# Kernel optimization log

Hardware: AMD Instinct MI355X
Metric: run time of the kernel (lower is better)

Reference implementation:

```python
import jax, jax.numpy as jnp
import numpy as np

B, V, H, E, Q = 32768, 2048, 256, 16, 4  # batch, num_visible, hidden_dim, num_experts, num_qubits
ENERGY_SCALE = 3.0
T_INIT, T_FINAL, N_STEPS = 1.0, 0.1, 100
SEED = 1  # annealing_counter after one call


def setup_inputs() -> dict:
    key = jax.random.key(0)
    ks = jax.random.split(key, 6)
    x = jax.random.normal(ks[0], (B, V), jnp.float32)
    We = jax.random.normal(ks[1], (V, H), jnp.float32) / np.sqrt(V).astype(np.float32)
    be = jnp.zeros((H,), jnp.float32)
    W1 = jax.random.normal(ks[2], (H + E, Q), jnp.float32) / np.sqrt(H + E).astype(np.float32)
    b1 = jnp.zeros((Q,), jnp.float32)
    w2 = jax.random.normal(ks[3], (Q,), jnp.float32) / np.sqrt(Q).astype(np.float32)
    b2 = jnp.zeros((), jnp.float32)
    inv_temp = jnp.ones((), jnp.float32)  # initial_inverse_temp = 1.0
    return dict(x=x, We=We, be=be, W1=W1, b1=b1, w2=w2, b2=b2, inv_temp=inv_temp)


def _energies(x, We, be, W1, b1, w2, b2):
    # feature_encoder: Dense(H, tanh)
    enc = jnp.tanh(x @ We + be)                       # [B, H]
    # combined = concat([enc tiled over experts, one_hot(expert)], -1) -> energy MLP.
    # one_hot @ W1[H:] just selects rows, so split the matmul instead of tiling:
    W1e, W1i = W1[:H], W1[H:]                         # [H,Q], [E,Q]
    h = jnp.tanh(enc @ W1e[None] if False else jnp.tanh((enc @ W1e)[:, None, :] + W1i[None, :, :] + b1))  # [B,E,Q]
    energies = ENERGY_SCALE * jnp.tanh(jnp.einsum('beq,q->be', h, w2) + b2)  # [B, E]
    return energies


def _qbm_sample(energies, seed):
    # Annealed Metropolis-Hastings over experts, geometric temperature schedule.
    key = jax.random.key(seed)
    kinit, kloop = jax.random.split(key)
    cur = jax.random.randint(kinit, (B,), 0, E)
    log_ratio = jnp.log(jnp.float32(T_FINAL / T_INIT))

    def step(cur, t):
        kt = jax.random.fold_in(kloop, t)
        kp, ku = jax.random.split(kt)
        frac = t.astype(jnp.float32) / jnp.float32(N_STEPS - 1)
        T = jnp.float32(T_INIT) * jnp.exp(log_ratio * frac)
        prop = jax.random.randint(kp, (B,), 0, E)
        e_prop = jnp.take_along_axis(energies, prop[:, None], 1)[:, 0]
        e_cur = jnp.take_along_axis(energies, cur[:, None], 1)[:, 0]
        accept = jax.random.uniform(ku, (B,)) < jnp.exp(jnp.minimum((e_cur - e_prop) / T, 0.0) + 0.0) * jnp.exp(jnp.minimum(-(e_prop - e_cur) / T, 0.0) * 0.0)
        # standard MH: accept if u < exp(-dE/T) (auto-accepts dE<=0)
        accept = jax.random.uniform(jax.random.fold_in(ku, 1), (B,)) < jnp.exp(jnp.minimum(-(e_prop - e_cur) / T, 0.0))
        return jnp.where(accept, prop, cur), None

    cur, _ = jax.lax.scan(step, cur, jnp.arange(N_STEPS))
    logp = jax.nn.log_softmax(-energies / jnp.float32(T_FINAL), axis=-1)
    sample_log_probs = jnp.take_along_axis(logp, cur[:, None], 1)[:, 0]
    final_e = jnp.take_along_axis(energies, cur[:, None], 1)[:, 0]
    return cur, sample_log_probs, final_e


def reference(x, We, be, W1, b1, w2, b2, inv_temp):
    energies = _energies(x, We, be, W1, b1, w2, b2)   # [B, E]
    beta = jax.nn.softplus(inv_temp)
    logits = -beta * energies
    # training=True, use_annealing=True path: stochastic expert selection
    assignments, _slp, _ae = _qbm_sample(jax.lax.stop_gradient(energies), SEED)
    probabilities = jax.nn.one_hot(assignments, E, dtype=jnp.float32)
    return probabilities, energies, logits
```

## Files before the change

kernel.cpp:

```cpp
#include <hip/hip_runtime.h>
#include <math.h>
#include <stdint.h>

#define B_N 32768
#define V_N 2048
#define H_N 256
#define E_N 16
#define Q_N 4

#define KT 64
#define NSTRIP (V_N/KT)
#define BROWS 32
#define KG_N (V_N/8)
#define NSS (V_N/128)

#define RNG_PART 1

typedef double f64x4 __attribute__((ext_vector_type(4)));
typedef float  f32x4 __attribute__((ext_vector_type(4)));
typedef short  bf16x8 __attribute__((ext_vector_type(8)));

union U8 { unsigned u[4]; bf16x8 v; };

#define TF_R(x0,x1,r) { x0 += x1; x1 = ((x1 << (r)) | (x1 >> (32-(r)))); x1 ^= x0; }

__device__ __forceinline__ void tf_block(uint32_t k0, uint32_t k1, uint32_t &x0, uint32_t &x1){
  uint32_t k2 = k0 ^ k1 ^ 0x1BD11BDAu;
  x0 += k0; x1 += k1;
  TF_R(x0,x1,13) TF_R(x0,x1,15) TF_R(x0,x1,26) TF_R(x0,x1,6)
  x0 += k1; x1 += k2 + 1u;
  TF_R(x0,x1,17) TF_R(x0,x1,29) TF_R(x0,x1,16) TF_R(x0,x1,24)
  x0 += k2; x1 += k0 + 2u;
  TF_R(x0,x1,13) TF_R(x0,x1,15) TF_R(x0,x1,26) TF_R(x0,x1,6)
  x0 += k0; x1 += k1 + 3u;
  TF_R(x0,x1,17) TF_R(x0,x1,29) TF_R(x0,x1,16) TF_R(x0,x1,24)
  x0 += k1; x1 += k2 + 4u;
  TF_R(x0,x1,13) TF_R(x0,x1,15) TF_R(x0,x1,26) TF_R(x0,x1,6)
  x0 += k2; x1 += k0 + 5u;
}

__device__ __forceinline__ int run_kats(){
  uint32_t x0, x1;
  x0 = 0u; x1 = 0u;
  tf_block(0u, 0u, x0, x1);
  if (x0 != 0x6b200159u || x1 != 0x99ba4efeu) return 1;
  x0 = 0xFFFFFFFFu; x1 = 0xFFFFFFFFu;
  tf_block(0xFFFFFFFFu, 0xFFFFFFFFu, x0, x1);
  if (x0 != 0x1cb996fcu || x1 != 0xbb002be7u) return 2;
  x0 = 0x243f6a88u; x1 = 0x85a308d3u;
  tf_block(0x13198a2eu, 0x03707344u, x0, x1);
  if (x0 != 0xc4923a9cu || x1 != 0x483df7a0u) return 3;
  return 0;
}

__device__ __forceinline__ uint32_t rbits(uint32_t ka, uint32_t kb, uint32_t b){
#if RNG_PART
  uint32_t x0 = 0u, x1 = b;
  tf_block(ka, kb, x0, x1);
  return x0 ^ x1;
#else
  uint32_t i = b & 16383u;
  uint32_t x0 = i, x1 = i + 16384u;
  tf_block(ka, kb, x0, x1);
  return (b < 16384u) ? x0 : x1;
#endif
}

__device__ __forceinline__ double exp_pos_f64(double v){
  const double LOG2E  = 1.4426950408889634074;
  const double LN2HI  = 6.93147180369123816490e-01;
  const double LN2LO  = 1.90821492927058770002e-10;
  double k = rint(v * LOG2E);
  double r = fma(-k, LN2HI, v);
  r = fma(-k, LN2LO, r);
  double p = 1.6059043836821613e-10;
  p = fma(p, r, 2.08767569878681e-09);
  p = fma(p, r, 2.505210838544172e-08);
  p = fma(p, r, 2.7557319223985893e-07);
  p = fma(p, r, 2.755731922398589e-06);
  p = fma(p, r, 2.48015873015873e-05);
  p = fma(p, r, 1.984126984126984e-04);
  p = fma(p, r, 1.3888888888888889e-03);
  p = fma(p, r, 8.333333333333333e-03);
  p = fma(p, r, 4.1666666666666664e-02);
  p = fma(p, r, 1.6666666666666666e-01);
  p = fma(p, r, 5.0e-01);
  p = fma(p, r, 1.0);
  p = fma(p, r, 1.0);
  int n = (int)k;
  double sc = __longlong_as_double(((long long)(1023 + n)) << 52);
  return p * sc;
}

__device__ __forceinline__ double tanh_fast(double x){
  double ax = fabs(x);
  if (ax < 0.25){
    double z = x * x;
    double p = 9.691537956929451e-05;
    p = fma(p, z, -2.3912911424355248e-04);
    p = fma(p, z,  5.900274409455859e-04);
    p = fma(p, z, -1.4558343870513183e-03);
    p = fma(p, z,  3.592128036572481e-03);
    p = fma(p, z, -8.863235529902197e-03);
    p = fma(p, z,  2.1869488536155203e-02);
    p = fma(p, z, -5.396825396825397e-02);
    p = fma(p, z,  1.3333333333333333e-01);
    p = fma(p, z, -3.3333333333333333e-01);
    double q = fma(p, z, 1.0);
    return x * q;
  }
  if (ax > 19.0) return copysign(1.0, x);
  double y = exp_pos_f64(2.0 * ax);
  double t = 1.0 - 2.0/(y + 1.0);
  return copysign(t, x);
}

__device__ __forceinline__ double tanh_d(double x, unsigned slow){
  return slow ? tanh(x) : tanh_fast(x);
}

__device__ __forceinline__ unsigned cvt_pk_bf16(float a, float b){
  unsigned r;
  asm("v_cvt_pk_bf16_f32 %0, %1, %2" : "=v"(r) : "v"(a), "v"(b));
  return r;
}

template<bool CV>
__device__ __forceinline__ void splitpair(float a, float b, unsigned &uh, unsigned &um, unsigned &ul){
  float ha, hb, ma, mb;
  if (CV){
    uh = cvt_pk_bf16(a, b);
    ha = __uint_as_float(uh<<16); hb = __uint_as_float(uh & 0xFFFF0000u);
  } else {
    unsigned ua=__float_as_uint(a), ub=__float_as_uint(b);
    uh = (ua>>16) | (ub & 0xFFFF0000u);
    ha = __uint_as_float(ua & 0xFFFF0000u); hb = __uint_as_float(ub & 0xFFFF0000u);
  }
  float ra = a - ha, rb = b - hb;
  if (CV){
    um = cvt_pk_bf16(ra, rb);
    ma = __uint_as_float(um<<16); mb = __uint_as_float(um & 0xFFFF0000u);
  } else {
    unsigned va=__float_as_uint(ra), vb=__float_as_uint(rb);
    um = (va>>16) | (vb & 0xFFFF0000u);
    ma = __uint_as_float(va & 0xFFFF0000u); mb = __uint_as_float(vb & 0xFFFF0000u);
  }
  float sa = ra - ma, sb = rb - mb;
  if (CV) ul = cvt_pk_bf16(sa, sb);
  else    ul = (__float_as_uint(sa)>>16) | (__float_as_uint(sb) & 0xFFFF0000u);
}

template<bool CV>
__device__ __forceinline__ void split8(const float* v, bf16x8& fh, bf16x8& fm, bf16x8& fl){
  U8 H, M, L;
  #pragma unroll
  for (int p=0;p<4;++p)
    splitpair<CV>(v[2*p], v[2*p+1], H.u[p], M.u[p], L.u[p]);
  fh=H.v; fm=M.v; fl=L.v;
}

__device__ __forceinline__ float bslot(bf16x8 f, int j){
  return __uint_as_float(((unsigned)(unsigned short)f[j]) << 16);
}

__device__ __forceinline__ double Aref(int i, int k){ return 0.5 + 0.03*i - 0.7*k + 0.011*i*k; }
__device__ __forceinline__ double Bref(int k, int j){ return 1.1*k - 0.17*j + 0.019*j*k + 0.23; }
__device__ __forceinline__ int Aint(int i, int k){ return ((i*5 + k*3) % 13) - 6; }
__device__ __forceinline__ int Bint(int k, int j){ return ((k*7 + j*11) % 17) - 8; }

__global__ __launch_bounds__(1024) void s0_kernel(unsigned* __restrict__ wsu, float log_ratio,
                          const float* __restrict__ invt){
#pragma clang fp contract(off)
  __shared__ int sbad, sbadc, sbadt;
  int t = threadIdx.x;
  if (t == 0){ sbad = 0; sbadc = 0; sbadt = 0; }
  __syncthreads();

  {
    int bad = 0;
    for (int i = 0; i < 64; ++i){
      int idx = t * 64 + i;
      double x = -20.0 + 40.0 * ((double)idx + 0.5) / 65536.0;
      double a = tanh_fast(x);
      double b = tanh(x);
      if ((float)a != (float)b) bad = 1;
      long long ia = __double_as_longlong(a), ib = __double_as_longlong(b);
      long long d = ia - ib; if (d < 0) d = -d;
      if (d > 8) bad = 1;
    }
    if (bad) atomicOr(&sbad, 1);
  }

  {
    float xv[8];
    #pragma unroll
    for (int p=0;p<8;++p){
      unsigned idx = (unsigned)(t*8+p);
      unsigned mant = (idx * 2654435761u) & 0x7FFFFFu;
      unsigned ex = 127u + (idx*7u)%8u - 4u;
      unsigned sgn = (idx & 1u) << 31;
      xv[p] = __uint_as_float(sgn | (ex<<23) | mant);
    }
    bf16x8 h,m,l;
    int badc=0, badt=0;
    split8<true>(xv,h,m,l);
    #pragma unroll
    for (int p=0;p<8;++p){
      double s = (double)bslot(h,p)+(double)bslot(m,p)+(double)bslot(l,p);
      if (s != (double)xv[p]) badc=1;
      if (fabsf(bslot(m,p)) > fabsf(xv[p])*0.00784f) badc=1;
    }
    split8<false>(xv,h,m,l);
    #pragma unroll
    for (int p=0;p<8;++p){
      double s = (double)bslot(h,p)+(double)bslot(m,p)+(double)bslot(l,p);
      if (s != (double)xv[p]) badt=1;
    }
    if (badc) atomicOr(&sbadc, 1);
    if (badt) atomicOr(&sbadt, 1);
  }

  if (t < 64){
    int l = t;
    int lr = l & 15, g = l >> 4;
    {
      double aval = Aref(lr, g);
      double bval = Bref(g, lr);
      int found = 8;
      for (int combo = 0; combo < 8; ++combo){
        int swap = combo & 1, drow = (combo>>1)&1, dt = (combo>>2)&1;
        f64x4 c = {0.0,0.0,0.0,0.0};
        if (swap) c = __builtin_amdgcn_mfma_f64_16x16x4f64(bval, aval, c, 0,0,0);
        else      c = __builtin_amdgcn_mfma_f64_16x16x4f64(aval, bval, c, 0,0,0);
        int bad = 0;
        #pragma unroll
        for (int r=0;r<4;++r){
          int f = drow ? (g + 4*r) : (4*g + r);
          int row = dt ? lr : f;
          int col = dt ? f  : lr;
          double e = 0.0;
          #pragma unroll
          for (int k=0;k<4;++k) e += Aref(row,k)*Bref(k,col);
          if (fabs(c[r] - e) > 1e-9) bad = 1;
        }
        if (__ballot(bad != 0) == 0ull){ found = combo; break; }
      }
      if (l == 0) wsu[503] = (unsigned)found;
    }
    {
      bf16x8 af, bf;
      #pragma unroll
      for (int j=0;j<8;++j){
        af[j] = (short)(__float_as_uint((float)Aint(lr, g*8+j)) >> 16);
        bf[j] = (short)(__float_as_uint((float)Bint(g*8+j, lr)) >> 16);
      }
      int found = 8;
      for (int combo = 0; combo < 8; ++combo){
        int swap = combo & 1, drow = (combo>>1)&1, dt = (combo>>2)&1;
        f32x4 c = {0.f,0.f,0.f,0.f};
        if (swap) c = __builtin_amdgcn_mfma_f32_16x16x32_bf16(bf, af, c, 0,0,0);
        else      c = __builtin_amdgcn_mfma_f32_16x16x32_bf16(af, bf, c, 0,0,0);
        int bad = 0;
        #pragma unroll
        for (int r=0;r<4;++r){
          int f = drow ? (g + 4*r) : (4*g + r);
          int row = dt ? lr : f;
          int col = dt ? f  : lr;
          int e = 0;
          for (int k=0;k<32;++k) e += Aint(row,k)*Bint(k,col);
          if (c[r] != (float)e) bad = 1;
        }
        if (__ballot(bad != 0) == 0ull){ found = combo; break; }
      }
      if (l == 0) wsu[506] = (unsigned)found;
    }
  }
  __syncthreads();
  if (t == 0){
    wsu[504] = (unsigned)sbad;
    wsu[507] = sbadc ? (sbadt ? 2u : 1u) : 0u;
  }

  uint32_t ka = 0u, kb = 1u;
  uint32_t kinit0, kinit1, kl0, kl1;
#if RNG_PART
  { uint32_t a0=0u,a1=0u; tf_block(ka,kb,a0,a1); kinit0=a0; kinit1=a1; }
  { uint32_t a0=0u,a1=1u; tf_block(ka,kb,a0,a1); kl0=a0; kl1=a1; }
#else
  { uint32_t c00=0u,c01=2u; tf_block(ka,kb,c00,c01);
    uint32_t c10=1u,c11=3u; tf_block(ka,kb,c10,c11);
    kinit0=c00; kinit1=c10; kl0=c01; kl1=c11; }
#endif
  if (t == 0){
    wsu[502] = (unsigned)run_kats();
    wsu[505] = __float_as_uint(-(float)log1p(exp((double)invt[0])));
#if RNG_PART
    uint32_t x0=0u, x1=1u; tf_block(kinit0,kinit1,x0,x1);
    wsu[500]=x0; wsu[501]=x1;
#else
    uint32_t e00=0u,e01=2u; tf_block(kinit0,kinit1,e00,e01);
    uint32_t e10=1u,e11=3u; tf_block(kinit0,kinit1,e10,e11);
    wsu[500]=e01; wsu[501]=e11;
#endif
  }
  if (t < 100){
    uint32_t kt0=0u, kt1=(uint32_t)t; tf_block(kl0,kl1,kt0,kt1);
    uint32_t q0, q1, v0, v1;
#if RNG_PART
    uint32_t p0=0u,p1=0u; tf_block(kt0,kt1,p0,p1);
    uint32_t u0=0u,u1=1u; tf_block(kt0,kt1,u0,u1);
    { uint32_t a=0u,b=1u; tf_block(p0,p1,a,b); q0=a; q1=b; }
    { uint32_t a=0u,b=1u; tf_block(u0,u1,a,b); v0=a; v1=b; }
#else
    uint32_t d00=0u,d01=2u; tf_block(kt0,kt1,d00,d01);
    uint32_t d10=1u,d11=3u; tf_block(kt0,kt1,d10,d11);
    uint32_t kp0=d00, kp1=d10, ku0=d01, ku1k=d11;
    uint32_t e00=0u,e01=2u; tf_block(kp0,kp1,e00,e01);
    uint32_t e10=1u,e11=3u; tf_block(kp0,kp1,e10,e11);
    q0=e01; q1=e11;
    { uint32_t a=0u,b=1u; tf_block(ku0,ku1k,a,b); v0=a; v1=b; }
#endif
    float fr = (float)t / 99.0f;
    float arg = log_ratio * fr;
    float T = (float)exp((double)arg);
    wsu[t*5+0]=q0; wsu[t*5+1]=q1; wsu[t*5+2]=v0; wsu[t*5+3]=v1;
    wsu[t*5+4]=__float_as_uint(T);
  }
}

__global__ __launch_bounds__(256) void bsplit_kernel(
    const float* __restrict__ We, const unsigned* __restrict__ wsu,
    bf16x8* __restrict__ Bh, bf16x8* __restrict__ Bm, bf16x8* __restrict__ Bl){
#pragma clang fp contract(off)
  int kg = blockIdx.x;
  int col = threadIdx.x;
  float v[8];
  #pragma unroll
  for (int i=0;i<8;++i)
    v[i] = We[(size_t)(kg*8+i)*H_N + col];
  bf16x8 h, m, l;
  if (wsu[507] == 0u) split8<true >(v, h, m, l);
  else                split8<false>(v, h, m, l);
  size_t o = (size_t)kg*H_N + col;
  Bh[o] = h; Bm[o] = m; Bl[o] = l;
}

template<bool SWAP, bool CV>
__device__ __forceinline__ void bf16_gemm_lds(
    const float* __restrict__ x,
    const bf16x8* __restrict__ Bh, const bf16x8* __restrict__ Bm, const bf16x8* __restrict__ Bl,
    bf16x8* Ahs, bf16x8* Ams, bf16x8* Als,
    f32x4 c8[2][2], double hh64[2][2][4],
    int tid, int wave, int lr, int lk, int row0)
{
  f32x4 hh[2][2];
  #pragma unroll
  for (int rt=0;rt<2;++rt)
    #pragma unroll
    for (int j=0;j<2;++j){
      hh[rt][j] = (f32x4){0.f,0.f,0.f,0.f};
      c8[rt][j] = (f32x4){0.f,0.f,0.f,0.f};
      #pragma unroll
      for (int r=0;r<4;++r) hh64[rt][j][r] = 0.0;
    }

#define MMB(a,b,c) (SWAP ? __builtin_amdgcn_mfma_f32_16x16x32_bf16((b),(a),(c),0,0,0) \
                         : __builtin_amdgcn_mfma_f32_16x16x32_bf16((a),(b),(c),0,0,0))

  const int col0 = wave*32 + lr;
  const int col1 = col0 + 16;
  const int srow = tid >> 4;
  const int skg  = tid & 15;
  const float* xp = x + (size_t)(row0 + srow)*V_N + skg*8;

  for (int ss=0; ss<NSS; ++ss){
    {
      float v[8];
      *(float4*)(v)   = *(const float4*)(xp + ss*128);
      *(float4*)(v+4) = *(const float4*)(xp + ss*128 + 4);
      bf16x8 h, m, l;
      split8<CV>(v, h, m, l);
      Ahs[skg*33 + srow] = h;
      Ams[skg*33 + srow] = m;
      Als[skg*33 + srow] = l;
    }
    __syncthreads();

    #pragma unroll
    for (int half=0; half<2; ++half){
      #pragma unroll
      for (int kin2=0; kin2<2; ++kin2){
        const int kgl = (half*2 + kin2)*4 + lk;
        const int kg  = ss*16 + kgl;
        const size_t bbase = (size_t)kg*H_N;
        bf16x8 bh0 = Bh[bbase + col0];
        bf16x8 bm0 = Bm[bbase + col0];
        bf16x8 bl0 = Bl[bbase + col0];
        bf16x8 bh1 = Bh[bbase + col1];
        bf16x8 bm1 = Bm[bbase + col1];
        bf16x8 bl1 = Bl[bbase + col1];
        bf16x8 ah[2], am[2], al[2];
        ah[0] = Ahs[kgl*33 + lr];      am[0] = Ams[kgl*33 + lr];      al[0] = Als[kgl*33 + lr];
        ah[1] = Ahs[kgl*33 + 16 + lr]; am[1] = Ams[kgl*33 + 16 + lr]; al[1] = Als[kgl*33 + 16 + lr];
        #pragma unroll
        for (int rt=0;rt<2;++rt){
          hh[rt][0] = MMB(ah[rt], bh0, hh[rt][0]);
          c8[rt][0] = MMB(ah[rt], bm0, c8[rt][0]);
          c8[rt][0] = MMB(am[rt], bh0, c8[rt][0]);
          c8[rt][0] = MMB(ah[rt], bl0, c8[rt][0]);
          c8[rt][0] = MMB(am[rt], bm0, c8[rt][0]);
          c8[rt][0] = MMB(al[rt], bh0, c8[rt][0]);
          hh[rt][1] = MMB(ah[rt], bh1, hh[rt][1]);
          c8[rt][1] = MMB(ah[rt], bm1, c8[rt][1]);
          c8[rt][1] = MMB(am[rt], bh1, c8[rt][1]);
          c8[rt][1] = MMB(ah[rt], bl1, c8[rt][1]);
          c8[rt][1] = MMB(am[rt], bm1, c8[rt][1]);
          c8[rt][1] = MMB(al[rt], bh1, c8[rt][1]);
        }
      }
      #pragma unroll
      for (int rt=0;rt<2;++rt)
        #pragma unroll
        for (int j=0;j<2;++j){
          #pragma unroll
          for (int r=0;r<4;++r) hh64[rt][j][r] += (double)hh[rt][j][r];
          hh[rt][j] = (f32x4){0.f,0.f,0.f,0.f};
        }
    }
    __syncthreads();
  }
#undef MMB
}

template<bool SWAP, bool CV>
__device__ __forceinline__ void bf16_gemm(
    const float* __restrict__ x, const float* __restrict__ We,
    f32x4 c8[2][2], double hh64[2][2][4],
    int wave, int lr, int lk, int row0)
{
  f32x4 hh[2][2];
  #pragma unroll
  for (int rt=0;rt<2;++rt)
    #pragma unroll
    for (int j=0;j<2;++j){
      hh[rt][j] = (f32x4){0.f,0.f,0.f,0.f};
      c8[rt][j] = (f32x4){0.f,0.f,0.f,0.f};
      #pragma unroll
      for (int r=0;r<4;++r) hh64[rt][j][r] = 0.0;
    }

#define MMB(a,b,c) (SWAP ? __builtin_amdgcn_mfma_f32_16x16x32_bf16((b),(a),(c),0,0,0) \
                         : __builtin_amdgcn_mfma_f32_16x16x32_bf16((a),(b),(c),0,0,0))

  const float* xr0 = x + (size_t)(row0 + lr)*V_N + lk*8;
  const float* xr1 = x + (size_t)(row0 + 16 + lr)*V_N + lk*8;

  for (int s=0; s<NSTRIP; ++s){
    #pragma unroll
    for (int kin=0;kin<2;++kin){
      float bv0[8], bv1[8];
      const float* bp = We + ((size_t)(s*KT + kin*32 + lk*8))*H_N + wave*32 + lr;
      #pragma unroll
      for (int jj=0;jj<8;++jj){ bv0[jj] = bp[(size_t)jj*H_N]; bv1[jj] = bp[(size_t)jj*H_N + 16]; }
      bf16x8 bh0,bm0,bl0,bh1,bm1,bl1;
      split8<CV>(bv0, bh0, bm0, bl0);
      split8<CV>(bv1, bh1, bm1, bl1);
      bf16x8 ah[2], am[2], al[2];
      float av[8];
      *(float4*)(av)   = *(const float4*)(xr0 + s*KT + kin*32);
      *(float4*)(av+4) = *(const float4*)(xr0 + s*KT + kin*32 + 4);
      split8<CV>(av, ah[0], am[0], al[0]);
      *(float4*)(av)   = *(const float4*)(xr1 + s*KT + kin*32);
      *(float4*)(av+4) = *(const float4*)(xr1 + s*KT + kin*32 + 4);
      split8<CV>(av, ah[1], am[1], al[1]);
      #pragma unroll
      for (int rt=0;rt<2;++rt){
        hh[rt][0] = MMB(ah[rt], bh0, hh[rt][0]);
        c8[rt][0] = MMB(ah[rt], bm0, c8[rt][0]);
        c8[rt][0] = MMB(am[rt], bh0, c8[rt][0]);
        c8[rt][0] = MMB(ah[rt], bl0, c8[rt][0]);
        c8[rt][0] = MMB(am[rt], bm0, c8[rt][0]);
        c8[rt][0] = MMB(al[rt], bh0, c8[rt][0]);
        hh[rt][1] = MMB(ah[rt], bh1, hh[rt][1]);
        c8[rt][1] = MMB(ah[rt], bm1, c8[rt][1]);
        c8[rt][1] = MMB(am[rt], bh1, c8[rt][1]);
        c8[rt][1] = MMB(ah[rt], bl1, c8[rt][1]);
        c8[rt][1] = MMB(am[rt], bm1, c8[rt][1]);
        c8[rt][1] = MMB(al[rt], bh1, c8[rt][1]);
      }
    }
    #pragma unroll
    for (int rt=0;rt<2;++rt)
      #pragma unroll
      for (int j=0;j<2;++j){
        #pragma unroll
        for (int r=0;r<4;++r) hh64[rt][j][r] += (double)hh[rt][j][r];
        hh[rt][j] = (f32x4){0.f,0.f,0.f,0.f};
      }
  }
#undef MMB
}

template<bool SWAP>
__device__ __forceinline__ void mfma_strips(
    const float* __restrict__ x, const float* __restrict__ We,
    float* xs0, float* xs1, f64x4 acc[2][2],
    int tid, int wave, int lr, int lk, int row0)
{
  #pragma unroll
  for (int i=0;i<4;++i){
    int e = tid + i*512; int row = e >> 6; int k = e & 63;
    xs0[row*66 + k] = x[(size_t)(row0+row)*V_N + k];
  }
  __syncthreads();

  for (int s=0; s<NSTRIP; ++s){
    float* cur = (s & 1) ? xs1 : xs0;
    float* nxt = (s & 1) ? xs0 : xs1;

    float xr[4];
    if (s+1 < NSTRIP){
      #pragma unroll
      for (int i=0;i<4;++i){
        int e = tid + i*512; int row = e >> 6; int k = e & 63;
        xr[i] = x[(size_t)(row0+row)*V_N + (size_t)(s+1)*KT + k];
      }
    }

    const float* Bp = We + ((size_t)s*KT + lk)*H_N + wave*32 + lr;
    #pragma unroll 4
    for (int kk=0; kk<16; ++kk){
      double a0 = (double)cur[(     lr)*66 + kk*4 + lk];
      double a1 = (double)cur[(16 + lr)*66 + kk*4 + lk];
      #pragma unroll
      for (int j=0;j<2;++j){
        double bv = (double)Bp[j*16];
        if (SWAP){
          acc[0][j] = __builtin_amdgcn_mfma_f64_16x16x4f64(bv, a0, acc[0][j], 0,0,0);
          acc[1][j] = __builtin_amdgcn_mfma_f64_16x16x4f64(bv, a1, acc[1][j], 0,0,0);
        } else {
          acc[0][j] = __builtin_amdgcn_mfma_f64_16x16x4f64(a0, bv, acc[0][j], 0,0,0);
          acc[1][j] = __builtin_amdgcn_mfma_f64_16x16x4f64(a1, bv, acc[1][j], 0,0,0);
        }
      }
      Bp += 4*H_N;
    }

    if (s+1 < NSTRIP){
      #pragma unroll
      for (int i=0;i<4;++i){
        int e = tid + i*512; int row = e >> 6; int k = e & 63;
        nxt[row*66 + k] = xr[i];
      }
    }
    __syncthreads();
  }
}

__device__ __forceinline__ void valu_gemm_and_enc(
    const float* __restrict__ x, const float* __restrict__ We, const float* __restrict__ be,
    float* enc_s, int tid, int row0, unsigned slowtanh)
{
  const int rg = tid >> 6;
  const int c0 = (tid & 63) * 4;
  double acc[4][4];
  #pragma unroll
  for (int r=0;r<4;++r){ acc[r][0]=0.0; acc[r][1]=0.0; acc[r][2]=0.0; acc[r][3]=0.0; }

  for (int v=0; v<V_N; ++v){
    const float* wp = We + (size_t)v*H_N + c0;
    double w0=(double)wp[0], w1=(double)wp[1], w2d=(double)wp[2], w3=(double)wp[3];
    #pragma unroll
    for (int r4=0;r4<4;++r4){
      double xv = (double)x[(size_t)(row0+rg*4+r4)*V_N + v];
      acc[r4][0] = fma(xv, w0, acc[r4][0]);
      acc[r4][1] = fma(xv, w1, acc[r4][1]);
      acc[r4][2] = fma(xv, w2d, acc[r4][2]);
      acc[r4][3] = fma(xv, w3, acc[r4][3]);
    }
  }
  #pragma unroll
  for (int r4=0;r4<4;++r4){
    int r = rg*4 + r4;
    #pragma unroll
    for (int j=0;j<4;++j){
      int c = c0 + j;
      float m1 = (float)(acc[r4][j] + (double)be[c]);
      enc_s[r*257 + c] = (float)tanh_d((double)m1, slowtanh);
    }
  }
}

__global__ __launch_bounds__(512) void ke_kernel(
    const float* __restrict__ x, const float* __restrict__ We,
    const float* __restrict__ be, const float* __restrict__ W1,
    const float* __restrict__ b1, const float* __restrict__ w2,
    const float* __restrict__ b2, const float* __restrict__ invt,
    const unsigned* __restrict__ wsu,
    const bf16x8* __restrict__ Bh, const bf16x8* __restrict__ Bm,
    const bf16x8* __restrict__ Bl, int presplit,
    float* __restrict__ energ, float* __restrict__ logit,
    float* __restrict__ probs){
#pragma clang fp contract(off)
  __shared__ float smemf[BROWS*257];
  __shared__ double t2p[BROWS*4*4];
  __shared__ float t2_s[BROWS*4];
  float* xs0 = smemf;
  float* xs1 = smemf + BROWS*66;
  float* enc_s = smemf;
  float* en_s  = smemf;
  bf16x8* Ahs = (bf16x8*)smemf;
  bf16x8* Ams = Ahs + 16*33;
  bf16x8* Als = Ams + 16*33;

  const int tid = threadIdx.x;
  const int wave = tid >> 6;
  const int l = tid & 63;
  const int lr = l & 15;
  const int lk = l >> 4;
  const int row0 = blockIdx.x * BROWS;

  const unsigned combo64 = wsu[503];
  const unsigned combo16 = wsu[506];
  const unsigned splmode = wsu[507];
  const unsigned slowtanh = wsu[504];
  const unsigned katflag = wsu[502];
  const float nbeta = __uint_as_float(wsu[505]);

  if (combo16 < 8u && splmode < 2u){
    f32x4 c8[2][2];
    double hh64[2][2][4];
    const bool sw = (combo16 & 1u);
    if (presplit){
      if (splmode == 0u){
        if (sw) bf16_gemm_lds<true ,true >(x, Bh, Bm, Bl, Ahs, Ams, Als, c8, hh64, tid, wave, lr, lk, row0);
        else    bf16_gemm_lds<false,true >(x, Bh, Bm, Bl, Ahs, Ams, Als, c8, hh64, tid, wave, lr, lk, row0);
      } else {
        if (sw) bf16_gemm_lds<true ,false>(x, Bh, Bm, Bl, Ahs, Ams, Als, c8, hh64, tid, wave, lr, lk, row0);
        else    bf16_gemm_lds<false,false>(x, Bh, Bm, Bl, Ahs, Ams, Als, c8, hh64, tid, wave, lr, lk, row0);
      }
    } else if (splmode == 0u){
      if (sw) bf16_gemm<true ,true >(x, We, c8, hh64, wave, lr, lk, row0);
      else    bf16_gemm<false,true >(x, We, c8, hh64, wave, lr, lk, row0);
    } else {
      if (sw) bf16_gemm<true ,false>(x, We, c8, hh64, wave, lr, lk, row0);
      else    bf16_gemm<false,false>(x, We, c8, hh64, wave, lr, lk, row0);
    }
    __syncthreads();
    const int drow = (combo16 >> 1) & 1, dt = (combo16 >> 2) & 1;
    #pragma unroll
    for (int rt=0;rt<2;++rt){
      #pragma unroll
      for (int j=0;j<2;++j){
        #pragma unroll
        for (int r=0;r<4;++r){
          int f = drow ? (lk + 4*r) : (4*lk + r);
          int m = dt ? lr : f;
          int n = dt ? f  : lr;
          int row = rt*16 + m;
          int col = wave*32 + j*16 + n;
          double tot = hh64[rt][j][r] + (double)c8[rt][j][r] + (double)be[col];
          float m1 = (float)tot;
          enc_s[row*257 + col] = (float)tanh_d((double)m1, slowtanh);
        }
      }
    }
  } else if (combo64 < 8u){
    f64x4 acc[2][2];
    #pragma unroll
    for (int rt=0;rt<2;++rt)
      #pragma unroll
      for (int j=0;j<2;++j){ acc[rt][j][0]=0.0; acc[rt][j][1]=0.0; acc[rt][j][2]=0.0; acc[rt][j][3]=0.0; }
    if (combo64 & 1u) mfma_strips<true >(x, We, xs0, xs1, acc, tid, wave, lr, lk, row0);
    else              mfma_strips<false>(x, We, xs0, xs1, acc, tid, wave, lr, lk, row0);
    const int drow = (combo64 >> 1) & 1, dt = (combo64 >> 2) & 1;
    #pragma unroll
    for (int rt=0;rt<2;++rt){
      #pragma unroll
      for (int j=0;j<2;++j){
        #pragma unroll
        for (int r=0;r<4;++r){
          int f = drow ? (lk + 4*r) : (4*lk + r);
          int m = dt ? lr : f;
          int n = dt ? f  : lr;
          int row = rt*16 + m;
          int col = wave*32 + j*16 + n;
          float m1 = (float)(acc[rt][j][r] + (double)be[col]);
          enc_s[row*257 + col] = (float)tanh_d((double)m1, slowtanh);
        }
      }
    }
  } else {
    valu_gemm_and_enc(x, We, be, enc_s, tid, row0, slowtanh);
  }
  __syncthreads();

  {
    int r = tid >> 4, q = (tid >> 2) & 3, seg = tid & 3;
    double s = 0.0;
    const float* er = enc_s + r*257 + seg*64;
    const float* wq = W1 + seg*64*4 + q;
    #pragma unroll 8
    for (int hh=0; hh<64; ++hh)
      s = fma((double)er[hh], (double)wq[hh*4], s);
    t2p[(r*4+q)*4 + seg] = s;
  }
  __syncthreads();
  if (tid < 128){
    double s = ((t2p[tid*4+0] + t2p[tid*4+1]) + t2p[tid*4+2]) + t2p[tid*4+3];
    t2_s[tid] = (float)s;
  }
  __syncthreads();

  {
    int r = tid >> 4, e = tid & 15;
    float y = 0.0f;
    #pragma unroll
    for (int q=0;q<4;++q){
      float a1f = t2_s[r*4+q] + W1[(H_N+e)*4+q];
      float a2f = a1f + b1[q];
      float hin  = (float)tanh_d((double)a2f, slowtanh);
      float hout = (float)tanh_d((double)hin, slowtanh);
      y = y + hout * w2[q];
    }
    float yb = y + b2[0];
    float en = 3.0f * (float)tanh_d((double)yb, slowtanh);
    size_t gi = (size_t)(row0 + r)*E_N + e;
    energ[gi] = en;
    logit[gi] = nbeta * en;
    en_s[r*16 + e] = en;
  }
  __syncthreads();

  if (tid < 32){
    const int row = tid;
    const uint32_t b = (uint32_t)(row0 + row);
    float* op = probs + (size_t)(row0 + row)*E_N;

    if (katflag != 0u){
      float c = 0.10f + 0.05f * (float)katflag;
      #pragma unroll
      for (int j0=0; j0<16; j0+=4){
        float4 r4; r4.x=c; r4.y=c; r4.z=c; r4.w=c;
        *(float4*)(op + j0) = r4;
      }
    } else {
      const float* se = en_s + row*16;
      uint32_t cur = rbits(wsu[500], wsu[501], b) & 15u;
      for (int t=0; t<100; ++t){
        uint32_t pa=wsu[t*5+0], pb=wsu[t*5+1], ua=wsu[t*5+2], ub=wsu[t*5+3];
        float T = __uint_as_float(wsu[t*5+4]);
        uint32_t prop = rbits(pa, pb, b) & 15u;
        uint32_t ru   = rbits(ua, ub, b);
        float u = __uint_as_float((ru >> 9) | 0x3f800000u) - 1.0f;
        float ec = se[(int)cur];
        float ep = se[(int)prop];
        float z = (-(ep - ec)) / T;
        z = fminf(z, 0.0f);
        float a = (float)exp((double)z);
        cur = (u < a) ? prop : cur;
      }
      #pragma unroll
      for (int j0=0; j0<16; j0+=4){
        float4 r4;
        r4.x = (cur == (uint32_t)(j0+0)) ? 1.0f : 0.0f;
        r4.y = (cur == (uint32_t)(j0+1)) ? 1.0f : 0.0f;
        r4.z = (cur == (uint32_t)(j0+2)) ? 1.0f : 0.0f;
        r4.w = (cur == (uint32_t)(j0+3)) ? 1.0f : 0.0f;
        *(float4*)(op + j0) = r4;
      }
    }
  }
}

extern "C" void kernel_launch(void* const* d_in, const int* in_sizes, int n_in,
                              void* d_out, int out_size, void* d_ws, size_t ws_size,
                              hipStream_t stream) {
  const float* x   = (const float*)d_in[0];
  const float* We  = (const float*)d_in[1];
  const float* be  = (const float*)d_in[2];
  const float* W1  = (const float*)d_in[3];
  const float* b1  = (const float*)d_in[4];
  const float* w2  = (const float*)d_in[5];
  const float* b2  = (const float*)d_in[6];
  const float* itp = (const float*)d_in[7];
  float* out = (float*)d_out;
  float* probs = out;
  float* energ = out + (size_t)B_N*E_N;
  float* logit = out + 2*(size_t)B_N*E_N;
  unsigned* wsu = (unsigned*)d_ws;

  const size_t bsz = (size_t)KG_N * H_N * 16;
  const size_t need = 4096 + 3*bsz;
  int presplit = (ws_size >= need) ? 1 : 0;
  char* base = (char*)d_ws + 4096;
  bf16x8* Bh = (bf16x8*)(base);
  bf16x8* Bm = (bf16x8*)(base + bsz);
  bf16x8* Bl = (bf16x8*)(base + 2*bsz);

  float log_ratio = (float)log((double)((float)0.1));

  hipLaunchKernelGGL(s0_kernel, dim3(1), dim3(1024), 0, stream, wsu, log_ratio, itp);
  if (presplit)
    hipLaunchKernelGGL(bsplit_kernel, dim3(KG_N), dim3(256), 0, stream, We, wsu, Bh, Bm, Bl);
  hipLaunchKernelGGL(ke_kernel, dim3(B_N/BROWS), dim3(512), 0, stream,
                     x, We, be, W1, b1, w2, b2, itp, wsu,
                     Bh, Bm, Bl, presplit,
                     energ, logit, probs);
}
```

Measured before the change: 490.7 us.

## Split annealed MH sampling out of encoder kernel into separate sampling kernel

Moves the 100-step Metropolis-Hastings sampling loop out of the fused GEMM/energy kernel, where only 32 of 512 threads ran it serially after the energies were computed, into a dedicated kernel with one thread per batch row. The sampling kernel reads energies back from global memory into LDS and writes the one-hot probabilities. This removes the serial tail from the heavy GEMM blocks, so they can retire sooner and occupancy improves. The cost is an extra launch and a round trip of the energies through global memory.

Measured after the change: 461.8 us. 1.06x faster.

```diff
diff --git a/kernel.cpp b/kernel.cpp
--- a/kernel.cpp
+++ b/kernel.cpp
@@ -599,8 +599,7 @@
     const unsigned* __restrict__ wsu,
     const bf16x8* __restrict__ Bh, const bf16x8* __restrict__ Bm,
     const bf16x8* __restrict__ Bl, int presplit,
-    float* __restrict__ energ, float* __restrict__ logit,
-    float* __restrict__ probs){
+    float* __restrict__ energ, float* __restrict__ logit){
 #pragma clang fp contract(off)
   __shared__ float smemf[BROWS*257];
   __shared__ double t2p[BROWS*4*4];
@@ -608,7 +607,6 @@
   float* xs0 = smemf;
   float* xs1 = smemf + BROWS*66;
   float* enc_s = smemf;
-  float* en_s  = smemf;
   bf16x8* Ahs = (bf16x8*)smemf;
   bf16x8* Ams = Ahs + 16*33;
   bf16x8* Als = Ams + 16*33;
@@ -624,7 +622,6 @@
   const unsigned combo16 = wsu[506];
   const unsigned splmode = wsu[507];
   const unsigned slowtanh = wsu[504];
-  const unsigned katflag = wsu[502];
   const float nbeta = __uint_as_float(wsu[505]);
 
   if (combo16 < 8u && splmode < 2u){
@@ -728,48 +725,58 @@
     size_t gi = (size_t)(row0 + r)*E_N + e;
     energ[gi] = en;
     logit[gi] = nbeta * en;
-    en_s[r*16 + e] = en;
-  }
-  __syncthreads();
-
-  if (tid < 32){
-    const int row = tid;
-    const uint32_t b = (uint32_t)(row0 + row);
-    float* op = probs + (size_t)(row0 + row)*E_N;
-
-    if (katflag != 0u){
-      float c = 0.10f + 0.05f * (float)katflag;
-      #pragma unroll
-      for (int j0=0; j0<16; j0+=4){
-        float4 r4; r4.x=c; r4.y=c; r4.z=c; r4.w=c;
-        *(float4*)(op + j0) = r4;
-      }
-    } else {
-      const float* se = en_s + row*16;
-      uint32_t cur = rbits(wsu[500], wsu[501], b) & 15u;
-      for (int t=0; t<100; ++t){
-        uint32_t pa=wsu[t*5+0], pb=wsu[t*5+1], ua=wsu[t*5+2], ub=wsu[t*5+3];
-        float T = __uint_as_float(wsu[t*5+4]);
-        uint32_t prop = rbits(pa, pb, b) & 15u;
-        uint32_t ru   = rbits(ua, ub, b);
-        float u = __uint_as_float((ru >> 9) | 0x3f800000u) - 1.0f;
-        float ec = se[(int)cur];
-        float ep = se[(int)prop];
-        float z = (-(ep - ec)) / T;
-        z = fminf(z, 0.0f);
-        float a = (float)exp((double)z);
-        cur = (u < a) ? prop : cur;
-      }
-      #pragma unroll
-      for (int j0=0; j0<16; j0+=4){
-        float4 r4;
-        r4.x = (cur == (uint32_t)(j0+0)) ? 1.0f : 0.0f;
-        r4.y = (cur == (uint32_t)(j0+1)) ? 1.0f : 0.0f;
-        r4.z = (cur == (uint32_t)(j0+2)) ? 1.0f : 0.0f;
-        r4.w = (cur == (uint32_t)(j0+3)) ? 1.0f : 0.0f;
-        *(float4*)(op + j0) = r4;
-      }
-    }
+  }
+}
+
+__global__ __launch_bounds__(128) void samp_kernel(
+    const float* __restrict__ energ, const unsigned* __restrict__ wsu,
+    float* __restrict__ probs){
+#pragma clang fp contract(off)
+  __shared__ float se[128*16];
+  const int lt = threadIdx.x;
+  const int b = blockIdx.x*128 + lt;
+
+  unsigned flag = wsu[502];
+  if (flag != 0u){
+    float c = 0.10f + 0.05f * (float)flag;
+    float* op = probs + (size_t)b*E_N;
+    #pragma unroll
+    for (int j0=0; j0<16; j0+=4){
+      float4 r; r.x=c; r.y=c; r.z=c; r.w=c;
+      *(float4*)(op + j0) = r;
+    }
+    return;
+  }
+
+  float4* sv = (float4*)(se + lt*16);
+  const float4* er = (const float4*)(energ + (size_t)b*E_N);
+  sv[0]=er[0]; sv[1]=er[1]; sv[2]=er[2]; sv[3]=er[3];
+
+  uint32_t k20 = wsu[500], k21 = wsu[501];
+  uint32_t cur = rbits(k20, k21, (uint32_t)b) & 15u;
+
+  for (int t=0; t<100; ++t){
+    uint32_t pa=wsu[t*5+0], pb=wsu[t*5+1], ua=wsu[t*5+2], ub=wsu[t*5+3];
+    float T = __uint_as_float(wsu[t*5+4]);
+    uint32_t prop = rbits(pa, pb, (uint32_t)b) & 15u;
+    uint32_t ru   = rbits(ua, ub, (uint32_t)b);
+    float u = __uint_as_float((ru >> 9) | 0x3f800000u) - 1.0f;
+    float ec = se[lt*16 + (int)cur];
+    float ep = se[lt*16 + (int)prop];
+    float z = (-(ep - ec)) / T;
+    z = fminf(z, 0.0f);
+    float a = (float)exp((double)z);
+    cur = (u < a) ? prop : cur;
+  }
+  float* op = probs + (size_t)b*E_N;
+  #pragma unroll
+  for (int j0=0; j0<16; j0+=4){
+    float4 r;
+    r.x = (cur == (uint32_t)(j0+0)) ? 1.0f : 0.0f;
+    r.y = (cur == (uint32_t)(j0+1)) ? 1.0f : 0.0f;
+    r.z = (cur == (uint32_t)(j0+2)) ? 1.0f : 0.0f;
+    r.w = (cur == (uint32_t)(j0+3)) ? 1.0f : 0.0f;
+    *(float4*)(op + j0) = r;
   }
 }
 
@@ -806,5 +813,7 @@
   hipLaunchKernelGGL(ke_kernel, dim3(B_N/BROWS), dim3(512), 0, stream,
                      x, We, be, W1, b1, w2, b2, itp, wsu,
                      Bh, Bm, Bl, presplit,
-                     energ, logit, probs);
-}
+                     energ, logit);
+  hipLaunchKernelGGL(samp_kernel, dim3(B_N/128), dim3(128), 0, stream,
+                     energ, wsu, probs);
+}
```

## Merge setup kernels, drop FP64 MFMA path, parallelize MH random generation

Applied to the files above, without the earlier changes.

Folds the weight-split kernel into the setup kernel as extra blocks, with each extra block recomputing the split-mode probe locally. This saves one launch and removes the dependency on wsu written by block 0. Deletes the unused FP64 MFMA GEMM fallback. The Threefry proposal and uniform draws for all 100 annealing steps are now generated by all 512 threads into shared memory, so the 32 serial Metropolis threads only do lookups instead of hashing. This uses more shared memory and duplicates the probe work in each extra block.

Result: faster. 431.8 us (median of 2 runs) (-12.0%).

```diff
diff --git a/kernel.cpp b/kernel.cpp
--- a/kernel.cpp
+++ b/kernel.cpp
@@ -8,8 +8,6 @@
 #define E_N 16
 #define Q_N 4
 
-#define KT 64
-#define NSTRIP (V_N/KT)
 #define BROWS 32
 #define KG_N (V_N/8)
 #define NSS (V_N/128)
@@ -163,18 +161,67 @@
   return __uint_as_float(((unsigned)(unsigned short)f[j]) << 16);
 }
 
+__device__ __forceinline__ float gate_val(unsigned idx){
+  unsigned mant = (idx * 2654435761u) & 0x7FFFFFu;
+  unsigned ex = 127u + (idx*7u)%8u - 4u;
+  unsigned sgn = (idx & 1u) << 31;
+  return __uint_as_float(sgn | (ex<<23) | mant);
+}
+
 __device__ __forceinline__ double Aref(int i, int k){ return 0.5 + 0.03*i - 0.7*k + 0.011*i*k; }
 __device__ __forceinline__ double Bref(int k, int j){ return 1.1*k - 0.17*j + 0.019*j*k + 0.23; }
 __device__ __forceinline__ int Aint(int i, int k){ return ((i*5 + k*3) % 13) - 6; }
 __device__ __forceinline__ int Bint(int k, int j){ return ((k*7 + j*11) % 17) - 8; }
 
-__global__ __launch_bounds__(1024) void s0_kernel(unsigned* __restrict__ wsu, float log_ratio,
-                          const float* __restrict__ invt){
+__global__ __launch_bounds__(1024) void init_kernel(unsigned* __restrict__ wsu, float log_ratio,
+    const float* __restrict__ invt, const float* __restrict__ We,
+    bf16x8* __restrict__ Bh, bf16x8* __restrict__ Bm, bf16x8* __restrict__ Bl, int presplit){
 #pragma clang fp contract(off)
   __shared__ int sbad, sbadc, sbadt;
   int t = threadIdx.x;
   if (t == 0){ sbad = 0; sbadc = 0; sbadt = 0; }
   __syncthreads();
+
+  if (blockIdx.x != 0){
+    if (!presplit) return;
+    {
+      float xv[8];
+      #pragma unroll
+      for (int p=0;p<8;++p) xv[p] = gate_val((unsigned)(t*8+p));
+      bf16x8 h,m,l;
+      int badc=0, badt=0;
+      split8<true>(xv,h,m,l);
+      #pragma unroll
+      for (int p=0;p<8;++p){
+        double s = (double)bslot(h,p)+(double)bslot(m,p)+(double)bslot(l,p);
+        if (s != (double)xv[p]) badc=1;
+        if (fabsf(bslot(m,p)) > fabsf(xv[p])*0.00784f) badc=1;
+      }
+      split8<false>(xv,h,m,l);
+      #pragma unroll
+      for (int p=0;p<8;++p){
+        double s = (double)bslot(h,p)+(double)bslot(m,p)+(double)bslot(l,p);
+        if (s != (double)xv[p]) badt=1;
+      }
+      if (badc) atomicOr(&sbadc, 1);
+      if (badt) atomicOr(&sbadt, 1);
+    }
+    __syncthreads();
+    unsigned spl = sbadc ? (sbadt ? 2u : 1u) : 0u;
+    if (spl >= 2u) return;
+    int kg = (blockIdx.x - 1)*4 + (t >> 8);
+    int col = t & 255;
+    float v[8];
+    #pragma unroll
+    for (int i=0;i<8;++i)
+      v[i] = We[(size_t)(kg*8+i)*H_N + col];
+    bf16x8 h, m, l;
+    if (spl == 0u) split8<true >(v, h, m, l);
+    else           split8<false>(v, h, m, l);
+    size_t o = (size_t)kg*H_N + col;
+    Bh[o] = h; Bm[o] = m; Bl[o] = l;
+    return;
+  }
 
   {
     int bad = 0;
@@ -194,13 +241,7 @@
   {
     float xv[8];
     #pragma unroll
-    for (int p=0;p<8;++p){
-      unsigned idx = (unsigned)(t*8+p);
-      unsigned mant = (idx * 2654435761u) & 0x7FFFFFu;
-      unsigned ex = 127u + (idx*7u)%8u - 4u;
-      unsigned sgn = (idx & 1u) << 31;
-      xv[p] = __uint_as_float(sgn | (ex<<23) | mant);
-    }
+    for (int p=0;p<8;++p) xv[p] = gate_val((unsigned)(t*8+p));
     bf16x8 h,m,l;
     int badc=0, badt=0;
     split8<true>(xv,h,m,l);
@@ -326,23 +367,6 @@
     wsu[t*5+0]=q0; wsu[t*5+1]=q1; wsu[t*5+2]=v0; wsu[t*5+3]=v1;
     wsu[t*5+4]=__float_as_uint(T);
   }
-}
-
-__global__ __launch_bounds__(256) void bsplit_kernel(
-    const float* __restrict__ We, const unsigned* __restrict__ wsu,
-    bf16x8* __restrict__ Bh, bf16x8* __restrict__ Bm, bf16x8* __restrict__ Bl){
-#pragma clang fp contract(off)
-  int kg = blockIdx.x;
-  int col = threadIdx.x;
-  float v[8];
-  #pragma unroll
-  for (int i=0;i<8;++i)
-    v[i] = We[(size_t)(kg*8+i)*H_N + col];
-  bf16x8 h, m, l;
-  if (wsu[507] == 0u) split8<true >(v, h, m, l);
-  else                split8<false>(v, h, m, l);
-  size_t o = (size_t)kg*H_N + col;
-  Bh[o] = h; Bm[o] = m; Bl[o] = l;
 }
 
 template<bool SWAP, bool CV>
@@ -455,11 +479,11 @@
   const float* xr0 = x + (size_t)(row0 + lr)*V_N + lk*8;
   const float* xr1 = x + (size_t)(row0 + 16 + lr)*V_N + lk*8;
 
-  for (int s=0; s<NSTRIP; ++s){
+  for (int s=0; s<32; ++s){
     #pragma unroll
     for (int kin=0;kin<2;++kin){
       float bv0[8], bv1[8];
-      const float* bp = We + ((size_t)(s*KT + kin*32 + lk*8))*H_N + wave*32 + lr;
+      const float* bp = We + ((size_t)(s*64 + kin*32 + lk*8))*H_N + wave*32 + lr;
       #pragma unroll
       for (int jj=0;jj<8;++jj){ bv0[jj] = bp[(size_t)jj*H_N]; bv1[jj] = bp[(size_t)jj*H_N + 16]; }
       bf16x8 bh0,bm0,bl0,bh1,bm1,bl1;
@@ -467,11 +491,11 @@
       split8<CV>(bv1, bh1, bm1, bl1);
       bf16x8 ah[2], am[2], al[2];
       float av[8];
-      *(float4*)(av)   = *(const float4*)(xr0 + s*KT + kin*32);
-      *(float4*)(av+4) = *(const float4*)(xr0 + s*KT + kin*32 + 4);
+      *(float4*)(av)   = *(const float4*)(xr0 + s*64 + kin*32);
+      *(float4*)(av+4) = *(const float4*)(xr0 + s*64 + kin*32 + 4);
       split8<CV>(av, ah[0], am[0], al[0]);
-      *(float4*)(av)   = *(const float4*)(xr1 + s*KT + kin*32);
-      *(float4*)(av+4) = *(const float4*)(xr1 + s*KT + kin*32 + 4);
+      *(float4*)(av)   = *(const float4*)(xr1 + s*64 + kin*32);
+      *(float4*)(av+4) = *(const float4*)(xr1 + s*64 + kin*32 + 4);
       split8<CV>(av, ah[1], am[1], al[1]);
       #pragma unroll
       for (int rt=0;rt<2;++rt){
@@ -499,62 +523,6 @@
       }
   }
 #undef MMB
-}
-
-template<bool SWAP>
-__device__ __forceinline__ void mfma_strips(
-    const float* __restrict__ x, const float* __restrict__ We,
-    float* xs0, float* xs1, f64x4 acc[2][2],
-    int tid, int wave, int lr, int lk, int row0)
-{
-  #pragma unroll
-  for (int i=0;i<4;++i){
-    int e = tid + i*512; int row = e >> 6; int k = e & 63;
-    xs0[row*66 + k] = x[(size_t)(row0+row)*V_N + k];
-  }
-  __syncthreads();
-
-  for (int s=0; s<NSTRIP; ++s){
-    float* cur = (s & 1) ? xs1 : xs0;
-    float* nxt = (s & 1) ? xs0 : xs1;
-
-    float xr[4];
-    if (s+1 < NSTRIP){
-      #pragma unroll
-      for (int i=0;i<4;++i){
-        int e = tid + i*512; int row = e >> 6; int k = e & 63;
-        xr[i] = x[(size_t)(row0+row)*V_N + (size_t)(s+1)*KT + k];
-      }
-    }
-
-    const float* Bp = We + ((size_t)s*KT + lk)*H_N + wave*32 + lr;
-    #pragma unroll 4
-    for (int kk=0; kk<16; ++kk){
-      double a0 = (double)cur[(     lr)*66 + kk*4 + lk];
-      double a1 = (double)cur[(16 + lr)*66 + kk*4 + lk];
-      #pragma unroll
-      for (int j=0;j<2;++j){
-        double bv = (double)Bp[j*16];
-        if (SWAP){
-          acc[0][j] = __builtin_amdgcn_mfma_f64_16x16x4f64(bv, a0, acc[0][j], 0,0,0);
-          acc[1][j] = __builtin_amdgcn_mfma_f64_16x16x4f64(bv, a1, acc[1][j], 0,0,0);
-        } else {
-          acc[0][j] = __builtin_amdgcn_mfma_f64_16x16x4f64(a0, bv, acc[0][j], 0,0,0);
-          acc[1][j] = __builtin_amdgcn_mfma_f64_16x16x4f64(a1, bv, acc[1][j], 0,0,0);
-        }
-      }
-      Bp += 4*H_N;
-    }
-
-    if (s+1 < NSTRIP){
-      #pragma unroll
-      for (int i=0;i<4;++i){
-        int e = tid + i*512; int row = e >> 6; int k = e & 63;
-        nxt[row*66 + k] = xr[i];
-      }
-    }
-    __syncthreads();
-  }
 }
 
 __device__ __forceinline__ void valu_gemm_and_enc(
@@ -605,13 +573,13 @@
   __shared__ float smemf[BROWS*257];
   __shared__ double t2p[BROWS*4*4];
   __shared__ float t2_s[BROWS*4];
-  float* xs0 = smemf;
-  float* xs1 = smemf + BROWS*66;
   float* enc_s = smemf;
-  float* en_s  = smemf;
   bf16x8* Ahs = (bf16x8*)smemf;
   bf16x8* Ams = Ahs + 16*33;
   bf16x8* Als = Ams + 16*33;
+  float* en_s = smemf;
+  float* us   = smemf + 512;
+  unsigned* ps = (unsigned*)(smemf + 3712);
 
   const int tid = threadIdx.x;
   const int wave = tid >> 6;
@@ -620,7 +588,6 @@
   const int lk = l >> 4;
   const int row0 = blockIdx.x * BROWS;
 
-  const unsigned combo64 = wsu[503];
   const unsigned combo16 = wsu[506];
   const unsigned splmode = wsu[507];
   const unsigned slowtanh = wsu[504];
@@ -665,31 +632,6 @@
         }
       }
     }
-  } else if (combo64 < 8u){
-    f64x4 acc[2][2];
-    #pragma unroll
-    for (int rt=0;rt<2;++rt)
-      #pragma unroll
-      for (int j=0;j<2;++j){ acc[rt][j][0]=0.0; acc[rt][j][1]=0.0; acc[rt][j][2]=0.0; acc[rt][j][3]=0.0; }
-    if (combo64 & 1u) mfma_strips<true >(x, We, xs0, xs1, acc, tid, wave, lr, lk, row0);
-    else              mfma_strips<false>(x, We, xs0, xs1, acc, tid, wave, lr, lk, row0);
-    const int drow = (combo64 >> 1) & 1, dt = (combo64 >> 2) & 1;
-    #pragma unroll
-    for (int rt=0;rt<2;++rt){
-      #pragma unroll
-      for (int j=0;j<2;++j){
-        #pragma unroll
-        for (int r=0;r<4;++r){
-          int f = drow ? (lk + 4*r) : (4*lk + r);
-          int m = dt ? lr : f;
-          int n = dt ? f  : lr;
-          int row = rt*16 + m;
-          int col = wave*32 + j*16 + n;
-          float m1 = (float)(acc[rt][j][r] + (double)be[col]);
-          enc_s[row*257 + col] = (float)tanh_d((double)m1, slowtanh);
-        }
-      }
-    }
   } else {
     valu_gemm_and_enc(x, We, be, enc_s, tid, row0, slowtanh);
   }
@@ -730,13 +672,23 @@
     logit[gi] = nbeta * en;
     en_s[r*16 + e] = en;
   }
+
+  if (katflag == 0u){
+    for (int i = tid; i < 3200; i += 512){
+      int t = i >> 5;
+      int row = i & 31;
+      uint32_t b = (uint32_t)(row0 + row);
+      uint32_t prop = rbits(wsu[t*5+0], wsu[t*5+1], b) & 15u;
+      uint32_t ru   = rbits(wsu[t*5+2], wsu[t*5+3], b);
+      us[t*32 + row] = __uint_as_float((ru >> 9) | 0x3f800000u) - 1.0f;
+      ps[t*32 + row] = prop;
+    }
+  }
   __syncthreads();
 
   if (tid < 32){
     const int row = tid;
-    const uint32_t b = (uint32_t)(row0 + row);
     float* op = probs + (size_t)(row0 + row)*E_N;
-
     if (katflag != 0u){
       float c = 0.10f + 0.05f * (float)katflag;
       #pragma unroll
@@ -746,13 +698,11 @@
       }
     } else {
       const float* se = en_s + row*16;
-      uint32_t cur = rbits(wsu[500], wsu[501], b) & 15u;
+      uint32_t cur = rbits(wsu[500], wsu[501], (uint32_t)(row0 + row)) & 15u;
       for (int t=0; t<100; ++t){
-        uint32_t pa=wsu[t*5+0], pb=wsu[t*5+1], ua=wsu[t*5+2], ub=wsu[t*5+3];
         float T = __uint_as_float(wsu[t*5+4]);
-        uint32_t prop = rbits(pa, pb, b) & 15u;
-        uint32_t ru   = rbits(ua, ub, b);
-        float u = __uint_as_float((ru >> 9) | 0x3f800000u) - 1.0f;
+        uint32_t prop = ps[t*32 + row];
+        float u = us[t*32 + row];
         float ec = se[(int)cur];
         float ep = se[(int)prop];
         float z = (-(ep - ec)) / T;
@@ -800,9 +750,8 @@
 
   float log_ratio = (float)log((double)((float)0.1));
 
-  hipLaunchKernelGGL(s0_kernel, dim3(1), dim3(1024), 0, stream, wsu, log_ratio, itp);
-  if (presplit)
-    hipLaunchKernelGGL(bsplit_kernel, dim3(KG_N), dim3(256), 0, stream, We, wsu, Bh, Bm, Bl);
+  hipLaunchKernelGGL(init_kernel, dim3(65), dim3(1024), 0, stream,
+                     wsu, log_ratio, itp, We, Bh, Bm, Bl, presplit);
   hipLaunchKernelGGL(ke_kernel, dim3(B_N/BROWS), dim3(512), 0, stream,
                      x, We, be, W1, b1, w2, b2, itp, wsu,
                      Bh, Bm, Bl, presplit,
```
